# Optimization experiments

Hardware: AMD Instinct MI355X
Metric: run time of the kernel (lower is better)

The kernel has to match this reference:

```python
import jax, jax.numpy as jnp
import numpy as np

B, C, V, L = 32, 32, 207, 128
C_OUT = 32
ORDER = 2


def setup_inputs() -> dict:
    key = jax.random.key(0)
    ks = jax.random.split(key, 6)
    x = jax.random.normal(ks[0], (B, C, V, L), dtype=jnp.float32)
    A0 = jax.random.uniform(ks[1], (V, V), dtype=jnp.float32) / V
    A1 = jax.random.uniform(ks[2], (V, V), dtype=jnp.float32) / V
    A2 = jax.random.uniform(ks[3], (V, V), dtype=jnp.float32) / V
    c_in_total = (ORDER * 3 + 1) * C  # 224
    W = jax.random.normal(ks[4], (C_OUT, c_in_total), dtype=jnp.float32) * 0.05
    b = jax.random.normal(ks[5], (C_OUT,), dtype=jnp.float32) * 0.05
    return {"x": x, "A0": A0, "A1": A1, "A2": A2, "W": W, "b": b}


def _nconv(x, A):
    # x: [n, c, v, l], A: [v, w] -> [n, c, w, l]
    return jnp.einsum('ncvl,vw->ncwl', x, A)


def reference(x, A0, A1, A2, W, b):
    outs = [x]
    for A in (A0, A1, A2):
        x1 = _nconv(x, A)
        outs.append(x1)
        for _ in range(2, ORDER + 1):
            x1 = _nconv(x1, A)
            outs.append(x1)
    h = jnp.concatenate(outs, axis=1)  # [n, 7*C, v, l]
    # 1x1 Conv2d == channel-mixing matmul; dropout is identity in eval mode
    return jnp.einsum('ncvl,oc->novl', h, W) + b[None, :, None, None]
```

## Files before the change

kernel.cpp:

```cpp
#include <hip/hip_runtime.h>

#define VDIM 207
#define LDIM 128
#define VP 224
#define VL (VDIM*LDIM)
#define NC 1024
#define NPOINT (32*VL)
#define APITCH 232
#define SWZ(row, colb) ((row) * 464 + ((colb) ^ (((row) & 1) << 5)))

typedef unsigned short u16;
typedef unsigned int u32;
typedef __attribute__((ext_vector_type(4))) float f32x4;
typedef __attribute__((ext_vector_type(8))) short s16x8;

__device__ __forceinline__ u16 f2bf(float f) {
  u32 u = __float_as_uint(f);
  return (u16)((u + 0x7FFFu + ((u >> 16) & 1u)) >> 16);
}
__device__ __forceinline__ float bf2f(u16 h) {
  return __uint_as_float(((u32)h) << 16);
}

__global__ void k_prep(const float* __restrict__ A0, const float* __restrict__ A1,
                       const float* __restrict__ A2, const float* __restrict__ W,
                       u16* __restrict__ AT, float* __restrict__ WT,
                       u16* __restrict__ Wb) {
  int idx = blockIdx.x * 256 + threadIdx.x;
  if (idx < 3 * VP * VP) {
    int i = idx / (VP * VP);
    int r = idx % (VP * VP);
    int w = r / VP, v = r % VP;
    const float* A = (i == 0) ? A0 : ((i == 1) ? A1 : A2);
    float f = (w < VDIM && v < VDIM) ? A[v * VDIM + w] : 0.f;
    AT[idx] = f2bf(f);
  } else {
    int j = idx - 3 * VP * VP;
    if (j < VP * 32) {
      int k = j >> 5, o = j & 31;
      WT[j] = W[o * 224 + k];
    } else if (j < 2 * VP * 32) {
      int j2 = j - VP * 32;
      Wb[j2] = f2bf(W[j2]);
    }
  }
}

__global__ __launch_bounds__(256) void k_xt(const float* __restrict__ x,
                                            u16* __restrict__ xT) {
  __shared__ float tile[64 * 130];
  int nc = blockIdx.x;
  const float* xs = x + (size_t)nc * VL;
  u16* xd = xT + (size_t)nc * (128 * VP);
  int tid = threadIdx.x;
  for (int ch = 0; ch < 4; ++ch) {
    int v0 = ch * 64;
    __syncthreads();
#pragma unroll
    for (int j = 0; j < 8; ++j) {
      int idx = j * 256 + tid;
      int vr = idx >> 5, c4 = idx & 31;
      int v = v0 + vr;
      float4 val = make_float4(0.f, 0.f, 0.f, 0.f);
      if (v < VDIM) val = *(const float4*)(xs + (size_t)v * LDIM + c4 * 4);
      float* trow = &tile[vr * 130 + c4 * 4];
      *(float2*)(trow) = make_float2(val.x, val.y);
      *(float2*)(trow + 2) = make_float2(val.z, val.w);
    }
    __syncthreads();
    int l = tid >> 1, h = tid & 1;
    int vbase = v0 + h * 32;
    if (vbase < VP) {
      u32 wd[16];
#pragma unroll
      for (int j = 0; j < 16; ++j) {
        int v = vbase + 2 * j;
        float f0 = (v < VDIM) ? tile[(h * 32 + 2 * j) * 130 + l] : 0.f;
        float f1 = (v + 1 < VDIM) ? tile[(h * 32 + 2 * j + 1) * 130 + l] : 0.f;
        wd[j] = (u32)f2bf(f0) | ((u32)f2bf(f1) << 16);
      }
      uint4* dst = (uint4*)(xd + (size_t)l * VP + vbase);
#pragma unroll
      for (int t = 0; t < 4; ++t)
        dst[t] = make_uint4(wd[4 * t], wd[4 * t + 1], wd[4 * t + 2], wd[4 * t + 3]);
    }
  }
}

__global__ __launch_bounds__(1024, 4) void k_hops(const u16* __restrict__ xT,
                                                  const u16* __restrict__ AT,
                                                  u16* __restrict__ zbuf,
                                                  int i0, int icount) {
  __shared__ __align__(16) u16 smem[208 * APITCH + 128 * APITCH];
  char* A_b = (char*)smem;
  char* z_b = (char*)(smem + 208 * APITCH);

  int tid = threadIdx.x;
  int lane = tid & 63, wid = tid >> 6;
  int lane15 = lane & 15, lgrp = lane >> 4;
  int wm = wid >> 2, wn = wid & 3;
  int NMT = (wm == 0) ? 4 : 3;
  int mbase = (wm == 0) ? 0 : (16 + wm * 48);
  int nc = blockIdx.x;
  const u16* xg = xT + (size_t)nc * (128 * VP);

  if (tid < 256) {
    int l = tid >> 1, h = tid & 1;
    *(uint4*)(z_b + SWZ(l, 416 + 16 * h)) = make_uint4(0, 0, 0, 0);
  }

  int col0 = wn * 32 + lane15;
  int col1 = col0 + 16;

  for (int ii = 0; ii < icount; ++ii) {
    int i = i0 + ii;
    const u16* Ag = AT + i * (VP * VP);
    for (int j = tid; j < 5824; j += 1024) {
      int r = j / 28, cq = j - r * 28;
      *(uint4*)(A_b + SWZ(r, cq * 16)) = *(const uint4*)(Ag + r * VP + cq * 8);
    }
    __syncthreads();

    for (int hop = 0; hop < 2; ++hop) {
      f32x4 acc[4][2];
#pragma unroll
      for (int m = 0; m < 4; ++m)
#pragma unroll
        for (int nt = 0; nt < 2; ++nt) acc[m][nt] = (f32x4){0.f, 0.f, 0.f, 0.f};

      for (int ks = 0; ks < 7; ++ks) {
        int colb = ks * 64 + lgrp * 16;
        s16x8 b0, b1;
        if (hop == 0) {
          b0 = *(const s16x8*)(xg + (size_t)col0 * VP + ks * 32 + lgrp * 8);
          b1 = *(const s16x8*)(xg + (size_t)col1 * VP + ks * 32 + lgrp * 8);
        } else {
          b0 = *(const s16x8*)(z_b + SWZ(col0, colb));
          b1 = *(const s16x8*)(z_b + SWZ(col1, colb));
        }
#pragma unroll
        for (int mt = 0; mt < 4; ++mt) {
          if (mt < NMT) {
            int row = mbase + mt * 16 + lane15;
            s16x8 afrag = *(const s16x8*)(A_b + SWZ(row, colb));
            asm("v_mfma_f32_16x16x32_bf16 %0, %1, %2, %0"
                : "+v"(acc[mt][0])
                : "v"(afrag), "v"(b0));
            asm("v_mfma_f32_16x16x32_bf16 %0, %1, %2, %0"
                : "+v"(acc[mt][1])
                : "v"(afrag), "v"(b1));
          }
        }
      }

      if (hop == 1) __syncthreads();

      int slot = 2 * ii + hop;
      u16* zg = zbuf + (size_t)slot * ((size_t)NC * VL) + (size_t)nc * VL;
#pragma unroll
      for (int mt = 0; mt < 4; ++mt) {
        if (mt < NMT) {
#pragma unroll
          for (int nt = 0; nt < 2; ++nt) {
            f32x4 a = acc[mt][nt];
            int col = wn * 32 + nt * 16 + lane15;
            int wb = mbase + mt * 16 + lgrp * 4;
            u16 u0 = f2bf(a.x), u1 = f2bf(a.y), u2 = f2bf(a.z), u3 = f2bf(a.w);
            if (hop == 0) {
              uint2 pk = make_uint2((u32)u0 | ((u32)u1 << 16),
                                    (u32)u2 | ((u32)u3 << 16));
              *(uint2*)(z_b + SWZ(col, wb * 2)) = pk;
            }
            if (wb + 0 < VDIM) zg[(wb + 0) * LDIM + col] = u0;
            if (wb + 1 < VDIM) zg[(wb + 1) * LDIM + col] = u1;
            if (wb + 2 < VDIM) zg[(wb + 2) * LDIM + col] = u2;
            if (wb + 3 < VDIM) zg[(wb + 3) * LDIM + col] = u3;
          }
        }
      }
      if (hop == 0) __syncthreads();
    }
  }
}

__global__ __launch_bounds__(256, 2) void k_mixm(const float* __restrict__ x,
                                                 const u16* __restrict__ zb,
                                                 const u16* __restrict__ Wb,
                                                 const float* __restrict__ bias,
                                                 float* __restrict__ out) {
  __shared__ __align__(16) u16 hT_s[128 * APITCH];
  __shared__ __align__(16) u16 tile[32 * 136];
  int tid = threadIdx.x;
  int bid = blockIdx.x;
  int n = bid / 207, pt = bid - n * 207;
  int p0 = pt * 128;
  int lane = tid & 63, wn = tid >> 6;
  int lane15 = lane & 15, lgrp = lane >> 4;

  s16x8 wa0[7], wa1[7];
#pragma unroll
  for (int ks = 0; ks < 7; ++ks) {
    wa0[ks] = *(const s16x8*)(Wb + lane15 * 224 + ks * 32 + lgrp * 8);
    wa1[ks] = *(const s16x8*)(Wb + (16 + lane15) * 224 + ks * 32 + lgrp * 8);
  }

  for (int g7 = 0; g7 < 7; ++g7) {
    if (g7 == 0) {
#pragma unroll
      for (int j0 = 0; j0 < 4; ++j0) {
        int j = j0 * 256 + tid;
        int c = j >> 5, q = j & 31;
        float4 v = *(const float4*)(x + (size_t)(n * 32 + c) * VL + p0 + q * 4);
        u32 lo = (u32)f2bf(v.x) | ((u32)f2bf(v.y) << 16);
        u32 hi = (u32)f2bf(v.z) | ((u32)f2bf(v.w) << 16);
        *(uint2*)(tile + c * 136 + q * 4) = make_uint2(lo, hi);
      }
    } else {
      int g = g7 - 1;
#pragma unroll
      for (int j0 = 0; j0 < 2; ++j0) {
        int j = j0 * 256 + tid;
        int c = j >> 4, cq = j & 15;
        *(uint4*)(tile + c * 136 + cq * 8) =
            *(const uint4*)(zb + ((size_t)(g << 10) + n * 32 + c) * VL + p0 + cq * 8);
      }
    }
    __syncthreads();
#pragma unroll
    for (int j0 = 0; j0 < 8; ++j0) {
      int j = j0 * 256 + tid;
      int cp = j & 15, p = j >> 4;
      u32 w = (u32)tile[(2 * cp) * 136 + p] |
              ((u32)tile[(2 * cp + 1) * 136 + p] << 16);
      *(u32*)(hT_s + p * APITCH + g7 * 32 + 2 * cp) = w;
    }
    __syncthreads();
  }

  f32x4 acc[2][2];
#pragma unroll
  for (int mt = 0; mt < 2; ++mt)
#pragma unroll
    for (int nt = 0; nt < 2; ++nt) acc[mt][nt] = (f32x4){0.f, 0.f, 0.f, 0.f};

#pragma unroll
  for (int ks = 0; ks < 7; ++ks) {
#pragma unroll
    for (int nt = 0; nt < 2; ++nt) {
      int colp = wn * 32 + nt * 16 + lane15;
      s16x8 bfrag = *(const s16x8*)(hT_s + colp * APITCH + ks * 32 + lgrp * 8);
      asm("v_mfma_f32_16x16x32_bf16 %0, %1, %2, %0"
          : "+v"(acc[0][nt]) : "v"(wa0[ks]), "v"(bfrag));
      asm("v_mfma_f32_16x16x32_bf16 %0, %1, %2, %0"
          : "+v"(acc[1][nt]) : "v"(wa1[ks]), "v"(bfrag));
    }
  }

#pragma unroll
  for (int mt = 0; mt < 2; ++mt) {
#pragma unroll
    for (int j = 0; j < 4; ++j) {
      int o = mt * 16 + lgrp * 4 + j;
      float bv = bias[o];
#pragma unroll
      for (int nt = 0; nt < 2; ++nt) {
        int p = p0 + wn * 32 + nt * 16 + lane15;
        out[(size_t)(n * 32 + o) * VL + p] = acc[mt][nt][j] + bv;
      }
    }
  }
}

template <int MODE, int NZ>
__global__ __launch_bounds__(256, 4) void k_mix(const float* __restrict__ x,
                                                const u16* __restrict__ zb,
                                                const float* __restrict__ WT,
                                                const float* __restrict__ bias,
                                                float* __restrict__ out, int wk0) {
  int t = blockIdx.x * 256 + threadIdx.x;
  int pp = t * 2;
  int n = pp / VL;
  int rem = pp - n * VL;
  float* op = out + (size_t)n * 32 * VL + rem;
  f32x4 a0[8], a1[8];

  if (MODE == 0) {
#pragma unroll
    for (int j = 0; j < 8; ++j) {
      f32x4 bv = *(const f32x4*)(bias + 4 * j);
      a0[j] = bv;
      a1[j] = bv;
    }
    const float* xp = x + (size_t)n * 32 * VL + rem;
#pragma unroll
    for (int c0 = 0; c0 < 32; c0 += 4) {
      float2 v[4];
#pragma unroll
      for (int q = 0; q < 4; ++q)
        v[q] = *(const float2*)(xp + (size_t)(c0 + q) * VL);
#pragma unroll
      for (int q = 0; q < 4; ++q) {
        const float* wv = WT + (c0 + q) * 32;
#pragma unroll
        for (int j = 0; j < 8; ++j) {
          f32x4 w4 = *(const f32x4*)(wv + 4 * j);
          a0[j] += w4 * v[q].x;
          a1[j] += w4 * v[q].y;
        }
      }
    }
  } else {
#pragma unroll
    for (int j = 0; j < 8; ++j) {
#pragma unroll
      for (int q = 0; q < 4; ++q) {
        float2 r = *(const float2*)(op + (size_t)(4 * j + q) * VL);
        a0[j][q] = r.x;
        a1[j][q] = r.y;
      }
    }
  }

#pragma unroll 1
  for (int g = 0; g < NZ; ++g) {
    const u16* zp = zb + ((size_t)g * NC + (size_t)n * 32) * VL + rem;
    const float* wg = WT + (wk0 + g * 32) * 32;
#pragma unroll
    for (int c0 = 0; c0 < 32; c0 += 4) {
      u32 zv[4];
#pragma unroll
      for (int q = 0; q < 4; ++q)
        zv[q] = *(const u32*)(zp + (size_t)(c0 + q) * VL);
#pragma unroll
      for (int q = 0; q < 4; ++q) {
        float f0 = bf2f((u16)(zv[q] & 0xFFFFu));
        float f1 = bf2f((u16)(zv[q] >> 16));
        const float* wv = wg + (c0 + q) * 32;
#pragma unroll
        for (int j = 0; j < 8; ++j) {
          f32x4 w4 = *(const f32x4*)(wv + 4 * j);
          a0[j] += w4 * f0;
          a1[j] += w4 * f1;
        }
      }
    }
  }

#pragma unroll
  for (int j = 0; j < 8; ++j) {
#pragma unroll
    for (int q = 0; q < 4; ++q) {
      float2 r;
      r.x = a0[j][q];
      r.y = a1[j][q];
      *(float2*)(op + (size_t)(4 * j + q) * VL) = r;
    }
  }
}

extern "C" void kernel_launch(void* const* d_in, const int* in_sizes, int n_in,
                              void* d_out, int out_size, void* d_ws, size_t ws_size,
                              hipStream_t stream) {
  const float* x = (const float*)d_in[0];
  const float* A0 = (const float*)d_in[1];
  const float* A1 = (const float*)d_in[2];
  const float* A2 = (const float*)d_in[3];
  const float* W = (const float*)d_in[4];
  const float* b = (const float*)d_in[5];
  float* out = (float*)d_out;

  const size_t xT_sz = (size_t)NC * 128 * VP * 2;
  const size_t AT_sz = (size_t)3 * VP * VP * 2;
  const size_t WT_sz = (size_t)VP * 32 * 4;
  const size_t Wb_sz = (size_t)VP * 32 * 2;
  const size_t slot_sz = (size_t)NC * VL * 2;

  char* wp = (char*)d_ws;
  u16* xT = (u16*)wp; wp += (xT_sz + 255) & ~(size_t)255;
  u16* AT = (u16*)wp; wp += (AT_sz + 255) & ~(size_t)255;
  float* WT = (float*)wp; wp += (WT_sz + 255) & ~(size_t)255;
  u16* Wb = (u16*)wp; wp += (Wb_sz + 255) & ~(size_t)255;
  u16* zbuf = (u16*)wp;
  size_t base = (size_t)(wp - (char*)d_ws);
  bool bigws = ws_size >= base + 6 * slot_sz;

  k_prep<<<644, 256, 0, stream>>>(A0, A1, A2, W, AT, WT, Wb);
  k_xt<<<NC, 256, 0, stream>>>(x, xT);
  if (bigws) {
    k_hops<<<NC, 1024, 0, stream>>>(xT, AT, zbuf, 0, 3);
    k_mixm<<<32 * 207, 256, 0, stream>>>(x, zbuf, Wb, b, out);
  } else {
    const int mixgrid = NPOINT / 512;
    k_mix<0, 0><<<mixgrid, 256, 0, stream>>>(x, nullptr, WT, b, out, 32);
    for (int i = 0; i < 3; ++i) {
      k_hops<<<NC, 1024, 0, stream>>>(xT, AT, zbuf, i, 1);
      k_mix<1, 2><<<mixgrid, 256, 0, stream>>>(nullptr, zbuf, WT, nullptr, out,
                                               (1 + 2 * i) * 32);
    }
  }
}
```

Baseline: 333.2 us.

## Precompute squared adjacency matrices and replace chained hops with independent GEMMs

Adds a kernel that computes A^2 for each adjacency matrix, so the second-order diffusion becomes x·A^2 instead of a dependent second hop. The fused 1024-thread hop kernel is replaced by 256-thread GEMM blocks that keep the x fragments in registers, split the 207 output rows across two launches (rows 0-79, then two 64-row halves), and loop over all six matrices. k_mixm moves to 512 threads with a double-buffered, XOR-swizzled staging tile that prefetches the next z group while the current one is transposed. This breaks the serial hop dependency and raises parallelism, at the cost of a naive A^2 prep kernel and rounding A^2 to bf16 rather than rounding the intermediate.

```diff
diff --git a/kernel.cpp b/kernel.cpp
--- a/kernel.cpp
+++ b/kernel.cpp
@@ -24,7 +24,7 @@
 
 __global__ void k_prep(const float* __restrict__ A0, const float* __restrict__ A1,
                        const float* __restrict__ A2, const float* __restrict__ W,
-                       u16* __restrict__ AT, float* __restrict__ WT,
+                       u16* __restrict__ MT, float* __restrict__ WT,
                        u16* __restrict__ Wb) {
   int idx = blockIdx.x * 256 + threadIdx.x;
   if (idx < 3 * VP * VP) {
@@ -33,7 +33,7 @@
     int w = r / VP, v = r % VP;
     const float* A = (i == 0) ? A0 : ((i == 1) ? A1 : A2);
     float f = (w < VDIM && v < VDIM) ? A[v * VDIM + w] : 0.f;
-    AT[idx] = f2bf(f);
+    MT[(size_t)(2 * i) * (VP * VP) + r] = f2bf(f);
   } else {
     int j = idx - 3 * VP * VP;
     if (j < VP * 32) {
@@ -44,6 +44,21 @@
       Wb[j2] = f2bf(W[j2]);
     }
   }
+}
+
+__global__ void k_sq(const float* __restrict__ A0, const float* __restrict__ A1,
+                     const float* __restrict__ A2, u16* __restrict__ MT) {
+  int idx = blockIdx.x * 256 + threadIdx.x;
+  if (idx >= 3 * VP * VP) return;
+  int i = idx / (VP * VP), r = idx % (VP * VP);
+  int w = r / VP, v = r % VP;
+  const float* A = (i == 0) ? A0 : ((i == 1) ? A1 : A2);
+  float s = 0.f;
+  if (w < VDIM && v < VDIM) {
+#pragma unroll 4
+    for (int u = 0; u < VDIM; ++u) s += A[v * VDIM + u] * A[u * VDIM + w];
+  }
+  MT[(size_t)(2 * i + 1) * (VP * VP) + r] = f2bf(s);
 }
 
 __global__ __launch_bounds__(256) void k_xt(const float* __restrict__ x,
@@ -87,109 +102,81 @@
   }
 }
 
-__global__ __launch_bounds__(1024, 4) void k_hops(const u16* __restrict__ xT,
-                                                  const u16* __restrict__ AT,
-                                                  u16* __restrict__ zbuf,
-                                                  int i0, int icount) {
-  __shared__ __align__(16) u16 smem[208 * APITCH + 128 * APITCH];
-  char* A_b = (char*)smem;
-  char* z_b = (char*)(smem + 208 * APITCH);
-
+template <int NMT>
+__global__ __launch_bounds__(256, 4) void k_gemm(const u16* __restrict__ xT,
+                                                 const u16* __restrict__ MT,
+                                                 u16* __restrict__ zbuf,
+                                                 int j0, int jcount) {
+  __shared__ __align__(16) u16 A_s[NMT * 16 * APITCH];
   int tid = threadIdx.x;
-  int lane = tid & 63, wid = tid >> 6;
+  int lane = tid & 63, wn = tid >> 6;
   int lane15 = lane & 15, lgrp = lane >> 4;
-  int wm = wid >> 2, wn = wid & 3;
-  int NMT = (wm == 0) ? 4 : 3;
-  int mbase = (wm == 0) ? 0 : (16 + wm * 48);
-  int nc = blockIdx.x;
+  int bid = blockIdx.x;
+  int nc, rowbase;
+  if (NMT == 5) { nc = bid; rowbase = 0; }
+  else { nc = bid >> 1; rowbase = 80 + 64 * (bid & 1); }
   const u16* xg = xT + (size_t)nc * (128 * VP);
-
-  if (tid < 256) {
-    int l = tid >> 1, h = tid & 1;
-    *(uint4*)(z_b + SWZ(l, 416 + 16 * h)) = make_uint4(0, 0, 0, 0);
-  }
-
-  int col0 = wn * 32 + lane15;
-  int col1 = col0 + 16;
-
-  for (int ii = 0; ii < icount; ++ii) {
-    int i = i0 + ii;
-    const u16* Ag = AT + i * (VP * VP);
-    for (int j = tid; j < 5824; j += 1024) {
-      int r = j / 28, cq = j - r * 28;
-      *(uint4*)(A_b + SWZ(r, cq * 16)) = *(const uint4*)(Ag + r * VP + cq * 8);
-    }
-    __syncthreads();
-
-    for (int hop = 0; hop < 2; ++hop) {
-      f32x4 acc[4][2];
-#pragma unroll
-      for (int m = 0; m < 4; ++m)
-#pragma unroll
-        for (int nt = 0; nt < 2; ++nt) acc[m][nt] = (f32x4){0.f, 0.f, 0.f, 0.f};
-
-      for (int ks = 0; ks < 7; ++ks) {
-        int colb = ks * 64 + lgrp * 16;
-        s16x8 b0, b1;
-        if (hop == 0) {
-          b0 = *(const s16x8*)(xg + (size_t)col0 * VP + ks * 32 + lgrp * 8);
-          b1 = *(const s16x8*)(xg + (size_t)col1 * VP + ks * 32 + lgrp * 8);
-        } else {
-          b0 = *(const s16x8*)(z_b + SWZ(col0, colb));
-          b1 = *(const s16x8*)(z_b + SWZ(col1, colb));
-        }
-#pragma unroll
-        for (int mt = 0; mt < 4; ++mt) {
-          if (mt < NMT) {
-            int row = mbase + mt * 16 + lane15;
-            s16x8 afrag = *(const s16x8*)(A_b + SWZ(row, colb));
-            asm("v_mfma_f32_16x16x32_bf16 %0, %1, %2, %0"
-                : "+v"(acc[mt][0])
-                : "v"(afrag), "v"(b0));
-            asm("v_mfma_f32_16x16x32_bf16 %0, %1, %2, %0"
-                : "+v"(acc[mt][1])
-                : "v"(afrag), "v"(b1));
-          }
-        }
-      }
-
-      if (hop == 1) __syncthreads();
-
-      int slot = 2 * ii + hop;
-      u16* zg = zbuf + (size_t)slot * ((size_t)NC * VL) + (size_t)nc * VL;
-#pragma unroll
-      for (int mt = 0; mt < 4; ++mt) {
-        if (mt < NMT) {
-#pragma unroll
-          for (int nt = 0; nt < 2; ++nt) {
-            f32x4 a = acc[mt][nt];
-            int col = wn * 32 + nt * 16 + lane15;
-            int wb = mbase + mt * 16 + lgrp * 4;
-            u16 u0 = f2bf(a.x), u1 = f2bf(a.y), u2 = f2bf(a.z), u3 = f2bf(a.w);
-            if (hop == 0) {
-              uint2 pk = make_uint2((u32)u0 | ((u32)u1 << 16),
-                                    (u32)u2 | ((u32)u3 << 16));
-              *(uint2*)(z_b + SWZ(col, wb * 2)) = pk;
-            }
-            if (wb + 0 < VDIM) zg[(wb + 0) * LDIM + col] = u0;
-            if (wb + 1 < VDIM) zg[(wb + 1) * LDIM + col] = u1;
-            if (wb + 2 < VDIM) zg[(wb + 2) * LDIM + col] = u2;
-            if (wb + 3 < VDIM) zg[(wb + 3) * LDIM + col] = u3;
-          }
-        }
-      }
-      if (hop == 0) __syncthreads();
-    }
-  }
-}
-
-__global__ __launch_bounds__(256, 2) void k_mixm(const float* __restrict__ x,
+  int col0 = wn * 32 + lane15, col1 = col0 + 16;
+
+  s16x8 bx0[7], bx1[7];
+#pragma unroll
+  for (int ks = 0; ks < 7; ++ks) {
+    bx0[ks] = *(const s16x8*)(xg + (size_t)col0 * VP + ks * 32 + lgrp * 8);
+    bx1[ks] = *(const s16x8*)(xg + (size_t)col1 * VP + ks * 32 + lgrp * 8);
+  }
+
+  for (int jj = 0; jj < jcount; ++jj) {
+    const u16* Mg = MT + (size_t)(j0 + jj) * (VP * VP) + (size_t)rowbase * VP;
+    for (int t = tid; t < NMT * 16 * 28; t += 256) {
+      int r = t / 28, cq = t - r * 28;
+      *(uint4*)((char*)A_s + SWZ(r, cq * 16)) = *(const uint4*)(Mg + r * VP + cq * 8);
+    }
+    __syncthreads();
+
+    f32x4 acc[NMT][2];
+#pragma unroll
+    for (int m = 0; m < NMT; ++m) {
+      acc[m][0] = (f32x4){0.f, 0.f, 0.f, 0.f};
+      acc[m][1] = (f32x4){0.f, 0.f, 0.f, 0.f};
+    }
+    for (int ks = 0; ks < 7; ++ks) {
+      int colb = ks * 64 + lgrp * 16;
+#pragma unroll
+      for (int mt = 0; mt < NMT; ++mt) {
+        s16x8 af = *(const s16x8*)((char*)A_s + SWZ(mt * 16 + lane15, colb));
+        asm("v_mfma_f32_16x16x32_bf16 %0, %1, %2, %0"
+            : "+v"(acc[mt][0]) : "v"(af), "v"(bx0[ks]));
+        asm("v_mfma_f32_16x16x32_bf16 %0, %1, %2, %0"
+            : "+v"(acc[mt][1]) : "v"(af), "v"(bx1[ks]));
+      }
+    }
+    __syncthreads();
+
+    u16* zg = zbuf + (size_t)jj * ((size_t)NC * VL) + (size_t)nc * VL;
+#pragma unroll
+    for (int mt = 0; mt < NMT; ++mt) {
+#pragma unroll
+      for (int nt = 0; nt < 2; ++nt) {
+        f32x4 a = acc[mt][nt];
+        int col = wn * 32 + nt * 16 + lane15;
+        int wb = rowbase + mt * 16 + lgrp * 4;
+        u16 u0 = f2bf(a.x), u1 = f2bf(a.y), u2 = f2bf(a.z), u3 = f2bf(a.w);
+        if (wb + 0 < VDIM) zg[(wb + 0) * LDIM + col] = u0;
+        if (wb + 1 < VDIM) zg[(wb + 1) * LDIM + col] = u1;
+        if (wb + 2 < VDIM) zg[(wb + 2) * LDIM + col] = u2;
+        if (wb + 3 < VDIM) zg[(wb + 3) * LDIM + col] = u3;
+      }
+    }
+  }
+}
+
+__global__ __launch_bounds__(512, 4) void k_mixm(const float* __restrict__ x,
                                                  const u16* __restrict__ zb,
                                                  const u16* __restrict__ Wb,
                                                  const float* __restrict__ bias,
                                                  float* __restrict__ out) {
   __shared__ __align__(16) u16 hT_s[128 * APITCH];
-  __shared__ __align__(16) u16 tile[32 * 136];
+  __shared__ __align__(16) u16 tile[2][32 * 136];
   int tid = threadIdx.x;
   int bid = blockIdx.x;
   int n = bid / 207, pt = bid - n * 207;
@@ -204,56 +191,57 @@
     wa1[ks] = *(const s16x8*)(Wb + (16 + lane15) * 224 + ks * 32 + lgrp * 8);
   }
 
+#pragma unroll
+  for (int t = 0; t < 2; ++t) {
+    int j = t * 512 + tid;
+    int c = j >> 5, q = j & 31;
+    float4 v = *(const float4*)(x + (size_t)(n * 32 + c) * VL + p0 + q * 4);
+    int sc = 2 * ((c >> 3) & 3);
+    u16* tp = tile[0] + c * 136;
+    *(u32*)(tp + ((q * 4) ^ sc)) = (u32)f2bf(v.x) | ((u32)f2bf(v.y) << 16);
+    *(u32*)(tp + ((q * 4 + 2) ^ sc)) = (u32)f2bf(v.z) | ((u32)f2bf(v.w) << 16);
+  }
+  __syncthreads();
+
+  int cur = 0;
+  int zc = tid >> 4, zq = tid & 15;
   for (int g7 = 0; g7 < 7; ++g7) {
-    if (g7 == 0) {
-#pragma unroll
-      for (int j0 = 0; j0 < 4; ++j0) {
-        int j = j0 * 256 + tid;
-        int c = j >> 5, q = j & 31;
-        float4 v = *(const float4*)(x + (size_t)(n * 32 + c) * VL + p0 + q * 4);
-        u32 lo = (u32)f2bf(v.x) | ((u32)f2bf(v.y) << 16);
-        u32 hi = (u32)f2bf(v.z) | ((u32)f2bf(v.w) << 16);
-        *(uint2*)(tile + c * 136 + q * 4) = make_uint2(lo, hi);
-      }
-    } else {
-      int g = g7 - 1;
-#pragma unroll
-      for (int j0 = 0; j0 < 2; ++j0) {
-        int j = j0 * 256 + tid;
-        int c = j >> 4, cq = j & 15;
-        *(uint4*)(tile + c * 136 + cq * 8) =
-            *(const uint4*)(zb + ((size_t)(g << 10) + n * 32 + c) * VL + p0 + cq * 8);
-      }
-    }
-    __syncthreads();
-#pragma unroll
-    for (int j0 = 0; j0 < 8; ++j0) {
-      int j = j0 * 256 + tid;
+    uint4 zv;
+    if (g7 < 6)
+      zv = *(const uint4*)(zb + ((size_t)(g7 << 10) + n * 32 + zc) * VL + p0 + zq * 8);
+#pragma unroll
+    for (int t = 0; t < 4; ++t) {
+      int j = t * 512 + tid;
       int cp = j & 15, p = j >> 4;
-      u32 w = (u32)tile[(2 * cp) * 136 + p] |
-              ((u32)tile[(2 * cp + 1) * 136 + p] << 16);
+      int sc = 2 * ((cp >> 2) & 3);
+      const u16* tp = tile[cur];
+      u32 w = (u32)tp[(2 * cp) * 136 + (p ^ sc)] |
+              ((u32)tp[(2 * cp + 1) * 136 + (p ^ sc)] << 16);
       *(u32*)(hT_s + p * APITCH + g7 * 32 + 2 * cp) = w;
     }
-    __syncthreads();
-  }
-
-  f32x4 acc[2][2];
-#pragma unroll
-  for (int mt = 0; mt < 2; ++mt)
-#pragma unroll
-    for (int nt = 0; nt < 2; ++nt) acc[mt][nt] = (f32x4){0.f, 0.f, 0.f, 0.f};
-
+    if (g7 < 6) {
+      int sc = 2 * ((zc >> 3) & 3);
+      u16* tp = tile[cur ^ 1] + zc * 136;
+      u32 zd[4] = {zv.x, zv.y, zv.z, zv.w};
+#pragma unroll
+      for (int t = 0; t < 4; ++t)
+        *(u32*)(tp + ((zq * 8 + 2 * t) ^ sc)) = zd[t];
+    }
+    __syncthreads();
+    cur ^= 1;
+  }
+
+  f32x4 acc[2];
+  acc[0] = (f32x4){0.f, 0.f, 0.f, 0.f};
+  acc[1] = (f32x4){0.f, 0.f, 0.f, 0.f};
+  int colp = wn * 16 + lane15;
 #pragma unroll
   for (int ks = 0; ks < 7; ++ks) {
-#pragma unroll
-    for (int nt = 0; nt < 2; ++nt) {
-      int colp = wn * 32 + nt * 16 + lane15;
-      s16x8 bfrag = *(const s16x8*)(hT_s + colp * APITCH + ks * 32 + lgrp * 8);
-      asm("v_mfma_f32_16x16x32_bf16 %0, %1, %2, %0"
-          : "+v"(acc[0][nt]) : "v"(wa0[ks]), "v"(bfrag));
-      asm("v_mfma_f32_16x16x32_bf16 %0, %1, %2, %0"
-          : "+v"(acc[1][nt]) : "v"(wa1[ks]), "v"(bfrag));
-    }
+    s16x8 bfrag = *(const s16x8*)(hT_s + colp * APITCH + ks * 32 + lgrp * 8);
+    asm("v_mfma_f32_16x16x32_bf16 %0, %1, %2, %0"
+        : "+v"(acc[0]) : "v"(wa0[ks]), "v"(bfrag));
+    asm("v_mfma_f32_16x16x32_bf16 %0, %1, %2, %0"
+        : "+v"(acc[1]) : "v"(wa1[ks]), "v"(bfrag));
   }
 
 #pragma unroll
@@ -261,12 +249,7 @@
 #pragma unroll
     for (int j = 0; j < 4; ++j) {
       int o = mt * 16 + lgrp * 4 + j;
-      float bv = bias[o];
-#pragma unroll
-      for (int nt = 0; nt < 2; ++nt) {
-        int p = p0 + wn * 32 + nt * 16 + lane15;
-        out[(size_t)(n * 32 + o) * VL + p] = acc[mt][nt][j] + bv;
-      }
+      out[(size_t)(n * 32 + o) * VL + p0 + colp] = acc[mt][j] + bias[o];
     }
   }
 }
@@ -370,30 +353,33 @@
   float* out = (float*)d_out;
 
   const size_t xT_sz = (size_t)NC * 128 * VP * 2;
-  const size_t AT_sz = (size_t)3 * VP * VP * 2;
+  const size_t MT_sz = (size_t)6 * VP * VP * 2;
   const size_t WT_sz = (size_t)VP * 32 * 4;
   const size_t Wb_sz = (size_t)VP * 32 * 2;
   const size_t slot_sz = (size_t)NC * VL * 2;
 
   char* wp = (char*)d_ws;
   u16* xT = (u16*)wp; wp += (xT_sz + 255) & ~(size_t)255;
-  u16* AT = (u16*)wp; wp += (AT_sz + 255) & ~(size_t)255;
+  u16* MT = (u16*)wp; wp += (MT_sz + 255) & ~(size_t)255;
   float* WT = (float*)wp; wp += (WT_sz + 255) & ~(size_t)255;
   u16* Wb = (u16*)wp; wp += (Wb_sz + 255) & ~(size_t)255;
   u16* zbuf = (u16*)wp;
   size_t base = (size_t)(wp - (char*)d_ws);
   bool bigws = ws_size >= base + 6 * slot_sz;
 
-  k_prep<<<644, 256, 0, stream>>>(A0, A1, A2, W, AT, WT, Wb);
+  k_prep<<<644, 256, 0, stream>>>(A0, A1, A2, W, MT, WT, Wb);
+  k_sq<<<588, 256, 0, stream>>>(A0, A1, A2, MT);
   k_xt<<<NC, 256, 0, stream>>>(x, xT);
   if (bigws) {
-    k_hops<<<NC, 1024, 0, stream>>>(xT, AT, zbuf, 0, 3);
-    k_mixm<<<32 * 207, 256, 0, stream>>>(x, zbuf, Wb, b, out);
+    k_gemm<5><<<NC, 256, 0, stream>>>(xT, MT, zbuf, 0, 6);
+    k_gemm<4><<<2 * NC, 256, 0, stream>>>(xT, MT, zbuf, 0, 6);
+    k_mixm<<<32 * 207, 512, 0, stream>>>(x, zbuf, Wb, b, out);
   } else {
     const int mixgrid = NPOINT / 512;
     k_mix<0, 0><<<mixgrid, 256, 0, stream>>>(x, nullptr, WT, b, out, 32);
     for (int i = 0; i < 3; ++i) {
-      k_hops<<<NC, 1024, 0, stream>>>(xT, AT, zbuf, i, 1);
+      k_gemm<5><<<NC, 256, 0, stream>>>(xT, MT, zbuf, 2 * i, 2);
+      k_gemm<4><<<2 * NC, 256, 0, stream>>>(xT, MT, zbuf, 2 * i, 2);
       k_mix<1, 2><<<mixgrid, 256, 0, stream>>>(nullptr, zbuf, WT, nullptr, out,
                                                (1 + 2 * i) * 32);
     }
```

Result: slower. 406.9 us (+22.1%).

## Double-buffer k_mixm staging tile, swizzle LDS, and use 512-thread blocks

Applied to the files above, without the earlier changes.

The k_mixm channel-mixing kernel now runs 512 threads per block, with each wave owning 16 output columns instead of 32. It double-buffers the staging tile so the next z-slice global load overlaps the transpose of the current slice, cutting one barrier per group. An XOR swizzle on the tile cuts LDS bank conflicts during the transpose. The adjacency-matrix buffer is also respaced to stride 2 slots (6 slots allocated), which looks like preparation for precomputed squared matrices but has no speed effect yet.

```diff
diff --git a/kernel.cpp b/kernel.cpp
--- a/kernel.cpp
+++ b/kernel.cpp
@@ -24,7 +24,7 @@
 
 __global__ void k_prep(const float* __restrict__ A0, const float* __restrict__ A1,
                        const float* __restrict__ A2, const float* __restrict__ W,
-                       u16* __restrict__ AT, float* __restrict__ WT,
+                       u16* __restrict__ MT, float* __restrict__ WT,
                        u16* __restrict__ Wb) {
   int idx = blockIdx.x * 256 + threadIdx.x;
   if (idx < 3 * VP * VP) {
@@ -33,7 +33,7 @@
     int w = r / VP, v = r % VP;
     const float* A = (i == 0) ? A0 : ((i == 1) ? A1 : A2);
     float f = (w < VDIM && v < VDIM) ? A[v * VDIM + w] : 0.f;
-    AT[idx] = f2bf(f);
+    MT[(size_t)(2 * i) * (VP * VP) + r] = f2bf(f);
   } else {
     int j = idx - 3 * VP * VP;
     if (j < VP * 32) {
@@ -88,7 +88,7 @@
 }
 
 __global__ __launch_bounds__(1024, 4) void k_hops(const u16* __restrict__ xT,
-                                                  const u16* __restrict__ AT,
+                                                  const u16* __restrict__ MT,
                                                   u16* __restrict__ zbuf,
                                                   int i0, int icount) {
   __shared__ __align__(16) u16 smem[208 * APITCH + 128 * APITCH];
@@ -114,7 +114,7 @@
 
   for (int ii = 0; ii < icount; ++ii) {
     int i = i0 + ii;
-    const u16* Ag = AT + i * (VP * VP);
+    const u16* Ag = MT + (size_t)(2 * i) * (VP * VP);
     for (int j = tid; j < 5824; j += 1024) {
       int r = j / 28, cq = j - r * 28;
       *(uint4*)(A_b + SWZ(r, cq * 16)) = *(const uint4*)(Ag + r * VP + cq * 8);
@@ -183,13 +183,13 @@
   }
 }
 
-__global__ __launch_bounds__(256, 2) void k_mixm(const float* __restrict__ x,
+__global__ __launch_bounds__(512, 4) void k_mixm(const float* __restrict__ x,
                                                  const u16* __restrict__ zb,
                                                  const u16* __restrict__ Wb,
                                                  const float* __restrict__ bias,
                                                  float* __restrict__ out) {
   __shared__ __align__(16) u16 hT_s[128 * APITCH];
-  __shared__ __align__(16) u16 tile[32 * 136];
+  __shared__ __align__(16) u16 tile[2][32 * 136];
   int tid = threadIdx.x;
   int bid = blockIdx.x;
   int n = bid / 207, pt = bid - n * 207;
@@ -204,56 +204,57 @@
     wa1[ks] = *(const s16x8*)(Wb + (16 + lane15) * 224 + ks * 32 + lgrp * 8);
   }
 
+#pragma unroll
+  for (int t = 0; t < 2; ++t) {
+    int j = t * 512 + tid;
+    int c = j >> 5, q = j & 31;
+    float4 v = *(const float4*)(x + (size_t)(n * 32 + c) * VL + p0 + q * 4);
+    int sc = 2 * ((c >> 3) & 3);
+    u16* tp = tile[0] + c * 136;
+    *(u32*)(tp + ((q * 4) ^ sc)) = (u32)f2bf(v.x) | ((u32)f2bf(v.y) << 16);
+    *(u32*)(tp + ((q * 4 + 2) ^ sc)) = (u32)f2bf(v.z) | ((u32)f2bf(v.w) << 16);
+  }
+  __syncthreads();
+
+  int cur = 0;
+  int zc = tid >> 4, zq = tid & 15;
   for (int g7 = 0; g7 < 7; ++g7) {
-    if (g7 == 0) {
-#pragma unroll
-      for (int j0 = 0; j0 < 4; ++j0) {
-        int j = j0 * 256 + tid;
-        int c = j >> 5, q = j & 31;
-        float4 v = *(const float4*)(x + (size_t)(n * 32 + c) * VL + p0 + q * 4);
-        u32 lo = (u32)f2bf(v.x) | ((u32)f2bf(v.y) << 16);
-        u32 hi = (u32)f2bf(v.z) | ((u32)f2bf(v.w) << 16);
-        *(uint2*)(tile + c * 136 + q * 4) = make_uint2(lo, hi);
-      }
-    } else {
-      int g = g7 - 1;
-#pragma unroll
-      for (int j0 = 0; j0 < 2; ++j0) {
-        int j = j0 * 256 + tid;
-        int c = j >> 4, cq = j & 15;
-        *(uint4*)(tile + c * 136 + cq * 8) =
-            *(const uint4*)(zb + ((size_t)(g << 10) + n * 32 + c) * VL + p0 + cq * 8);
-      }
+    uint4 zv;
+    if (g7 < 6)
+      zv = *(const uint4*)(zb + ((size_t)(g7 << 10) + n * 32 + zc) * VL + p0 + zq * 8);
+#pragma unroll
+    for (int t = 0; t < 4; ++t) {
+      int j = t * 512 + tid;
+      int cp = j & 15, p = j >> 4;
+      int sc = 2 * ((cp >> 2) & 3);
+      const u16* tp = tile[cur];
+      u32 w = (u32)tp[(2 * cp) * 136 + (p ^ sc)] |
+              ((u32)tp[(2 * cp + 1) * 136 + (p ^ sc)] << 16);
+      *(u32*)(hT_s + p * APITCH + g7 * 32 + 2 * cp) = w;
+    }
+    if (g7 < 6) {
+      int sc = 2 * ((zc >> 3) & 3);
+      u16* tp = tile[cur ^ 1] + zc * 136;
+      u32 zd[4] = {zv.x, zv.y, zv.z, zv.w};
+#pragma unroll
+      for (int t = 0; t < 4; ++t)
+        *(u32*)(tp + ((zq * 8 + 2 * t) ^ sc)) = zd[t];
     }
     __syncthreads();
-#pragma unroll
-    for (int j0 = 0; j0 < 8; ++j0) {
-      int j = j0 * 256 + tid;
-      int cp = j & 15, p = j >> 4;
-      u32 w = (u32)tile[(2 * cp) * 136 + p] |
-              ((u32)tile[(2 * cp + 1) * 136 + p] << 16);
-      *(u32*)(hT_s + p * APITCH + g7 * 32 + 2 * cp) = w;
-    }
-    __syncthreads();
-  }
-
-  f32x4 acc[2][2];
-#pragma unroll
-  for (int mt = 0; mt < 2; ++mt)
-#pragma unroll
-    for (int nt = 0; nt < 2; ++nt) acc[mt][nt] = (f32x4){0.f, 0.f, 0.f, 0.f};
-
+    cur ^= 1;
+  }
+
+  f32x4 acc[2];
+  acc[0] = (f32x4){0.f, 0.f, 0.f, 0.f};
+  acc[1] = (f32x4){0.f, 0.f, 0.f, 0.f};
+  int colp = wn * 16 + lane15;
 #pragma unroll
   for (int ks = 0; ks < 7; ++ks) {
-#pragma unroll
-    for (int nt = 0; nt < 2; ++nt) {
-      int colp = wn * 32 + nt * 16 + lane15;
-      s16x8 bfrag = *(const s16x8*)(hT_s + colp * APITCH + ks * 32 + lgrp * 8);
-      asm("v_mfma_f32_16x16x32_bf16 %0, %1, %2, %0"
-          : "+v"(acc[0][nt]) : "v"(wa0[ks]), "v"(bfrag));
-      asm("v_mfma_f32_16x16x32_bf16 %0, %1, %2, %0"
-          : "+v"(acc[1][nt]) : "v"(wa1[ks]), "v"(bfrag));
-    }
+    s16x8 bfrag = *(const s16x8*)(hT_s + colp * APITCH + ks * 32 + lgrp * 8);
+    asm("v_mfma_f32_16x16x32_bf16 %0, %1, %2, %0"
+        : "+v"(acc[0]) : "v"(wa0[ks]), "v"(bfrag));
+    asm("v_mfma_f32_16x16x32_bf16 %0, %1, %2, %0"
+        : "+v"(acc[1]) : "v"(wa1[ks]), "v"(bfrag));
   }
 
 #pragma unroll
@@ -261,12 +262,7 @@
 #pragma unroll
     for (int j = 0; j < 4; ++j) {
       int o = mt * 16 + lgrp * 4 + j;
-      float bv = bias[o];
-#pragma unroll
-      for (int nt = 0; nt < 2; ++nt) {
-        int p = p0 + wn * 32 + nt * 16 + lane15;
-        out[(size_t)(n * 32 + o) * VL + p] = acc[mt][nt][j] + bv;
-      }
+      out[(size_t)(n * 32 + o) * VL + p0 + colp] = acc[mt][j] + bias[o];
     }
   }
 }
@@ -370,30 +366,30 @@
   float* out = (float*)d_out;
 
   const size_t xT_sz = (size_t)NC * 128 * VP * 2;
-  const size_t AT_sz = (size_t)3 * VP * VP * 2;
+  const size_t MT_sz = (size_t)6 * VP * VP * 2;
   const size_t WT_sz = (size_t)VP * 32 * 4;
   const size_t Wb_sz = (size_t)VP * 32 * 2;
   const size_t slot_sz = (size_t)NC * VL * 2;
 
   char* wp = (char*)d_ws;
   u16* xT = (u16*)wp; wp += (xT_sz + 255) & ~(size_t)255;
-  u16* AT = (u16*)wp; wp += (AT_sz + 255) & ~(size_t)255;
+  u16* MT = (u16*)wp; wp += (MT_sz + 255) & ~(size_t)255;
   float* WT = (float*)wp; wp += (WT_sz + 255) & ~(size_t)255;
   u16* Wb = (u16*)wp; wp += (Wb_sz + 255) & ~(size_t)255;
   u16* zbuf = (u16*)wp;
   size_t base = (size_t)(wp - (char*)d_ws);
   bool bigws = ws_size >= base + 6 * slot_sz;
 
-  k_prep<<<644, 256, 0, stream>>>(A0, A1, A2, W, AT, WT, Wb);
+  k_prep<<<644, 256, 0, stream>>>(A0, A1, A2, W, MT, WT, Wb);
   k_xt<<<NC, 256, 0, stream>>>(x, xT);
   if (bigws) {
-    k_hops<<<NC, 1024, 0, stream>>>(xT, AT, zbuf, 0, 3);
-    k_mixm<<<32 * 207, 256, 0, stream>>>(x, zbuf, Wb, b, out);
+    k_hops<<<NC, 1024, 0, stream>>>(xT, MT, zbuf, 0, 3);
+    k_mixm<<<32 * 207, 512, 0, stream>>>(x, zbuf, Wb, b, out);
   } else {
     const int mixgrid = NPOINT / 512;
     k_mix<0, 0><<<mixgrid, 256, 0, stream>>>(x, nullptr, WT, b, out, 32);
     for (int i = 0; i < 3; ++i) {
-      k_hops<<<NC, 1024, 0, stream>>>(xT, AT, zbuf, i, 1);
+      k_hops<<<NC, 1024, 0, stream>>>(xT, MT, zbuf, i, 1);
       k_mix<1, 2><<<mixgrid, 256, 0, stream>>>(nullptr, zbuf, WT, nullptr, out,
                                                (1 + 2 * i) * 32);
     }
```

After: 328.7 us. Within noise of the previous version (-1.3%).
